# Optimization experiments

Measured on AMD Instinct MI355X. Metric: run time of the kernel, lower is better.

The kernel has to match this reference:

```python
import jax, jax.numpy as jnp
import numpy as np

D_MODEL = 1024
NUM_HEADS = 16
HEAD_DIM = D_MODEL // NUM_HEADS


def setup_inputs() -> dict:
    key = jax.random.key(0)
    ks = jax.random.split(key, 11)
    B, S, D = 2, 2048, D_MODEL
    scale = 1.0 / np.sqrt(D)
    inp = {
        "q": jax.random.normal(ks[0], (B, S, D), dtype=jnp.float32),
        "k": jax.random.normal(ks[1], (B, S, D), dtype=jnp.float32),
        "v": jax.random.normal(ks[2], (B, S, D), dtype=jnp.float32),
        # torch nn.Linear weights are [out, in]; y = x @ W.T + b
        "Wq": jax.random.normal(ks[3], (D, D), dtype=jnp.float32) * scale,
        "bq": jnp.zeros((D,), dtype=jnp.float32),
        "Wk": jax.random.normal(ks[4], (D, D), dtype=jnp.float32) * scale,
        "bk": jnp.zeros((D,), dtype=jnp.float32),
        "Wv": jax.random.normal(ks[5], (D, D), dtype=jnp.float32) * scale,
        "bv": jnp.zeros((D,), dtype=jnp.float32),
        "Wo": jax.random.normal(ks[6], (D, D), dtype=jnp.float32) * scale,
        "bo": jnp.zeros((D,), dtype=jnp.float32),
    }
    return inp


def _split_heads(x):
    B, S, D = x.shape
    return x.reshape(B, S, NUM_HEADS, HEAD_DIM).transpose(0, 2, 1, 3)  # [B,H,S,hd]


def reference(q, k, v, Wq, bq, Wk, bk, Wv, bv, Wo, bo):
    B, S, D = q.shape
    qh = _split_heads(q @ Wq.T + bq)
    kh = _split_heads(k @ Wk.T + bk)
    vh = _split_heads(v @ Wv.T + bv)
    # scores: [B,H,S,S], causal mask, softmax
    scores = jnp.einsum("bhqd,bhkd->bhqk", qh, kh) / jnp.sqrt(
        jnp.asarray(HEAD_DIM, dtype=qh.dtype))
    causal = jnp.tril(jnp.ones((S, S), dtype=bool))
    scores = jnp.where(causal[None, None], scores, -jnp.inf)
    attn = jax.nn.softmax(scores, axis=-1)
    out = jnp.einsum("bhqk,bhkd->bhqd", attn, vh)  # [B,H,S,hd]
    out = out.transpose(0, 2, 1, 3).reshape(B, S, D)
    return out @ Wo.T + bo
```

## Files before the change

kernel.cpp:

```cpp
#include <hip/hip_runtime.h>
#include <hip/hip_bf16.h>
#include <cstdint>
#include <cstddef>

typedef __bf16 bf16;
typedef __bf16 bf16x2 __attribute__((ext_vector_type(2)));
typedef __bf16 bf16x4 __attribute__((ext_vector_type(4)));
typedef __bf16 bf16x8 __attribute__((ext_vector_type(8)));
typedef float f32x4 __attribute__((ext_vector_type(4)));
typedef float f32x16 __attribute__((ext_vector_type(16)));
typedef unsigned int u32x4 __attribute__((ext_vector_type(4)));

#define S_LEN 2048
#define DM 1024
#define NH 16
#define HD 64
#define NQKV (4096 * 1024)
#define NW (1024 * 1024)
#define QK_SCALE 0.18033688011112042f

__device__ __forceinline__ void gload_lds16(const bf16* g, bf16* l) {
  __builtin_amdgcn_global_load_lds(
      (const __attribute__((address_space(1))) void*)g,
      (__attribute__((address_space(3))) void*)l, 16, 0, 0);
}

__device__ __forceinline__ unsigned packbf(float lo, float hi) {
  bf16x2 t;
  t[0] = (bf16)lo;
  t[1] = (bf16)hi;
  return __builtin_bit_cast(unsigned, t);
}

__device__ __forceinline__ void pl32swap(unsigned& a, unsigned& b) {
#if __has_builtin(__builtin_amdgcn_permlane32_swap)
  auto r = __builtin_amdgcn_permlane32_swap((int)a, (int)b, false, false);
  a = (unsigned)r[0];
  b = (unsigned)r[1];
#else
  asm volatile("v_permlane32_swap_b32 %0, %1" : "+v"(a), "+v"(b));
#endif
}

__global__ __launch_bounds__(256) void cvt_all(
    const float* __restrict__ q, const float* __restrict__ k, const float* __restrict__ v,
    const float* __restrict__ Wq, const float* __restrict__ Wk, const float* __restrict__ Wv,
    const float* __restrict__ Wo, bf16* __restrict__ out) {
  const size_t i = ((size_t)blockIdx.x * 256 + threadIdx.x) * 8;
  const float* src;
  size_t off;
  if (i < (size_t)NQKV) { src = q; off = i; }
  else if (i < 2ull * NQKV) { src = k; off = i - NQKV; }
  else if (i < 3ull * NQKV) { src = v; off = i - 2ull * NQKV; }
  else {
    const size_t j = i - 3ull * NQKV;
    if (j < (size_t)NW) { src = Wq; off = j; }
    else if (j < 2ull * NW) { src = Wk; off = j - NW; }
    else if (j < 3ull * NW) { src = Wv; off = j - 2ull * NW; }
    else { src = Wo; off = j - 3ull * NW; }
  }
  const float4 a = *(const float4*)(src + off);
  const float4 b = *(const float4*)(src + off + 4);
  bf16x8 o;
  o[0] = (bf16)a.x; o[1] = (bf16)a.y; o[2] = (bf16)a.z; o[3] = (bf16)a.w;
  o[4] = (bf16)b.x; o[5] = (bf16)b.y; o[6] = (bf16)b.z; o[7] = (bf16)b.w;
  *(bf16x8*)(out + i) = o;
}

template <int MODE>
__global__ __launch_bounds__(256, 3) void gemm_bt(
    const bf16* __restrict__ A, const bf16* __restrict__ W,
    const float* __restrict__ bias0, const float* __restrict__ bias1,
    const float* __restrict__ bias2, void* __restrict__ Out,
    int M, int N, int K, float scale) {
  __shared__ __align__(16) bf16 sm[3 * 2 * 128 * 32];
  const int tid = threadIdx.x;
  const int lane = tid & 63, w = tid >> 6;
  const int wr = w >> 1, wc = w & 1;
  const int r16 = lane & 15, grp = lane >> 4;

  int flat = blockIdx.y * gridDim.x + blockIdx.x;
  const int cpx = (gridDim.x * gridDim.y) >> 3;
  flat = (flat & 7) * cpx + (flat >> 3);
  const int m0 = (flat / gridDim.x) * 128;
  const int n0 = (flat % gridDim.x) * 128;

  const int seg = n0 >> 10;
  const bf16* Ab = (MODE == 3) ? A + (size_t)seg * NQKV : A;

  f32x4 acc[4][4] = {};

  int stG[2], stL[2];
#pragma unroll
  for (int j = 0; j < 2; ++j) {
    const int lin = j * 256 + tid;
    const int row = lin >> 2;
    const int ch = (lin & 3) ^ (row & 3);
    stG[j] = row * K + ch * 8;
    stL[j] = lin * 8;
  }

#define GSTAGE(t, s)                                                           \
  {                                                                            \
    const int k0_ = (t) << 5;                                                  \
    bf16* as_ = sm + (s) * 8192;                                               \
    bf16* bs_ = as_ + 4096;                                                    \
    _Pragma("unroll") for (int j = 0; j < 2; ++j) {                            \
      gload_lds16(&Ab[(size_t)m0 * K + k0_ + stG[j]], &as_[stL[j]]);           \
      gload_lds16(&W[(size_t)n0 * K + k0_ + stG[j]], &bs_[stL[j]]);            \
    }                                                                          \
  }

  const int nk = K >> 5;
  GSTAGE(0, 0)
  GSTAGE(1, 1)

  int cur = 0;
  for (int t = 0; t < nk; ++t) {
    if (t + 1 < nk) asm volatile("s_waitcnt vmcnt(4)" ::: "memory");
    else            asm volatile("s_waitcnt vmcnt(0)" ::: "memory");
    __builtin_amdgcn_s_barrier();

    if (t + 2 < nk) {
      int nxt = cur + 2; if (nxt >= 3) nxt -= 3;
      GSTAGE(t + 2, nxt)
    }

    const char* Asl = (const char*)(sm + cur * 8192);
    const char* Bsl = Asl + 8192;
    {
      bf16x8 af[4], bfr[4];
#pragma unroll
      for (int m = 0; m < 4; ++m) {
        const int row = wr * 64 + m * 16 + r16;
        af[m] = *(const bf16x8*)(Asl + row * 64 + ((grp * 16) ^ ((row & 3) << 4)));
      }
#pragma unroll
      for (int n = 0; n < 4; ++n) {
        const int row = wc * 64 + n * 16 + r16;
        bfr[n] = *(const bf16x8*)(Bsl + row * 64 + ((grp * 16) ^ ((row & 3) << 4)));
      }
#pragma unroll
      for (int m = 0; m < 4; ++m)
#pragma unroll
        for (int n = 0; n < 4; ++n)
          acc[m][n] = __builtin_amdgcn_mfma_f32_16x16x32_bf16(af[m], bfr[n], acc[m][n], 0, 0, 0);
    }
    ++cur; if (cur == 3) cur = 0;
  }
#undef GSTAGE

  const float* bp = (MODE == 3) ? (seg == 0 ? bias0 : (seg == 1 ? bias1 : bias2)) : bias0;
  const float sc = (MODE == 3) ? (seg == 0 ? scale : 1.0f) : scale;

  if (MODE == 3 && seg == 2) {
    __syncthreads();
    bf16* T = sm + w * (32 * 76);
    const int b = (m0 + wr * 64) >> 11;
    const int srow0 = (m0 + wr * 64) & 2047;
    bf16* base2 = (bf16*)Out + 2 * (size_t)NQKV;
#pragma unroll
    for (int p = 0; p < 2; ++p) {
#pragma unroll
      for (int nn = 0; nn < 2; ++nn) {
        const int n = 2 * p + nn;
#pragma unroll
        for (int mq = 0; mq < 4; ++mq)
#pragma unroll
          for (int r = 0; r < 4; ++r) {
            const int d_l = nn * 16 + r16;
            const int s_l = mq * 16 + grp * 4 + r;
            const int cs = (n0 + wc * 64 + n * 16 + r16) & 1023;
            T[d_l * 76 + s_l] = (bf16)(acc[mq][n][r] + bp[cs]);
          }
      }
      __syncthreads();
#pragma unroll
      for (int j = 0; j < 4; ++j) {
        const int d_l = j * 8 + (lane >> 3);
        const int scnk = lane & 7;
        const uint2 lo = *(const uint2*)&T[d_l * 76 + scnk * 8];
        const uint2 hi = *(const uint2*)&T[d_l * 76 + scnk * 8 + 4];
        const int cs = (n0 + wc * 64 + p * 32 + d_l) & 1023;
        const int hh = cs >> 6, dd = cs & 63;
        bf16* dst = base2 + ((size_t)(b * NH + hh) * HD + dd) * S_LEN + srow0 + scnk * 8;
        uint4 val; val.x = lo.x; val.y = lo.y; val.z = hi.x; val.w = hi.y;
        *(uint4*)dst = val;
      }
      __syncthreads();
    }
    return;
  }

#pragma unroll
  for (int m = 0; m < 4; ++m) {
#pragma unroll
    for (int n = 0; n < 4; ++n) {
#pragma unroll
      for (int r = 0; r < 4; ++r) {
        const int row = m0 + wr * 64 + m * 16 + grp * 4 + r;
        const int col = n0 + wc * 64 + n * 16 + r16;
        const int cs = col & 1023;
        const float v = (acc[m][n][r] + bp[cs]) * sc;
        if (MODE == 3) {
          const int b = row >> 11, s = row & 2047, h = cs >> 6, d = cs & 63;
          bf16* base = (bf16*)Out + (size_t)seg * NQKV;
          base[((size_t)(b * NH + h) * S_LEN + s) * HD + d] = (bf16)v;
        } else {
          ((float*)Out)[(size_t)row * N + col] = v;
        }
      }
    }
  }
}

__global__ __launch_bounds__(256, 3) void attn_fwd13(
    const bf16* __restrict__ Qh, const bf16* __restrict__ Kh,
    const bf16* __restrict__ Vt, bf16* __restrict__ AO) {
  __shared__ __align__(16) bf16 Kl[3][64 * 64];
  __shared__ __align__(16) bf16 Vl[3][64 * 64];

  const int tid = threadIdx.x;
  const int lane = tid & 63, w = tid >> 6;
  const int q31 = lane & 31, h = lane >> 5;
  const int qh = w >> 1, kh = w & 1;
  const int koff = kh << 5;

  const int bid = blockIdx.x;
  const int xcd = bid & 7;
  const int within = bid >> 3;
  const int bh = xcd * 4 + (within & 3);
  const int c = 31 - (within >> 2);

  const bf16* Qb = Qh + (size_t)bh * S_LEN * HD;
  const bf16* Kb = Kh + (size_t)bh * S_LEN * HD;
  const bf16* Vb = Vt + (size_t)bh * HD * S_LEN;

  int stK[2], stV[2], stL[2];
#pragma unroll
  for (int i = 0; i < 2; ++i) {
    const int lin = i * 256 + tid;
    const int row = lin >> 3;
    const int colb = (lin & 7) * 16;
    const int scol = colb ^ ((row & 7) << 4);
    stK[i] = row * HD + (scol >> 1);
    stV[i] = row * S_LEN + (scol >> 1);
    stL[i] = lin * 8;
  }
  const int swz = (q31 & 7) << 4;

#define STAGE(t, buf)                                                          \
  {                                                                            \
    const bf16* kb_ = Kb + (size_t)(t) * 64 * HD;                              \
    const bf16* vb_ = Vb + (t) * 64;                                           \
    _Pragma("unroll") for (int i = 0; i < 2; ++i) {                            \
      gload_lds16(kb_ + stK[i], &Kl[buf][stL[i]]);                             \
      gload_lds16(vb_ + stV[i], &Vl[buf][stL[i]]);                             \
    }                                                                          \
  }

  {
    const int q0 = c << 6;
    const int nt = c + 1;
    const int q0w = q0 + (qh << 5);
    const int qg = q0w + q31;
    const int nt_w = (w == 1) ? nt - 1 : nt;
    const bool maskw = (w == 0) || (w == 3);

    bf16x8 qf[4];
#pragma unroll
    for (int ks = 0; ks < 4; ++ks)
      qf[ks] = *(const bf16x8*)&Qb[(size_t)qg * HD + ks * 16 + 8 * h];

    f32x16 acc0 = {}, acc1 = {};
    float m = -1e30f, l = 0.f;

    STAGE(0, 0)
    if (nt > 1) STAGE(1, 1)

    int cur = 0;
    for (int kt = 0; kt < nt; ++kt) {
      if (kt + 1 < nt) asm volatile("s_waitcnt vmcnt(4)" ::: "memory");
      else             asm volatile("s_waitcnt vmcnt(0)" ::: "memory");
      __builtin_amdgcn_s_barrier();

      if (kt + 2 < nt) {
        int nxt = cur + 2; if (nxt >= 3) nxt -= 3;
        STAGE(kt + 2, nxt)
      }

      if (kt < nt_w) {
        const bf16* KlC = &Kl[cur][0];
        const bf16* VlC = &Vl[cur][0];

        bf16x8 kf[4];
#pragma unroll
        for (int ks = 0; ks < 4; ++ks) {
          const int cc = (32 * ks + 16 * h) ^ swz;
          kf[ks] = *(const bf16x8*)((const char*)KlC + (koff + q31) * 128 + cc);
        }

        f32x16 p0 = {};
        __builtin_amdgcn_s_setprio(1);
#pragma unroll
        for (int ks = 0; ks < 4; ++ks)
          p0 = __builtin_amdgcn_mfma_f32_32x32x16_bf16(kf[ks], qf[ks], p0, 0, 0, 0);
        __builtin_amdgcn_s_setprio(0);

        bf16x8 vf[4];
#pragma unroll
        for (int ks = 0; ks < 2; ++ks)
#pragma unroll
          for (int db = 0; db < 2; ++db) {
            const int cc = (64 * kh + 32 * ks + 16 * h) ^ swz;
            vf[ks * 2 + db] =
                *(const bf16x8*)((const char*)VlC + (db * 32 + q31) * 128 + cc);
          }

        if (maskw && kt == nt - 1) {
#pragma unroll
          for (int r = 0; r < 16; ++r) {
            const int key = (kt << 6) + koff + (r & 3) + 8 * (r >> 2) + 4 * h;
            if (key > qg) p0[r] = -1e30f;
          }
        }
        float t_[16];
#pragma unroll
        for (int r = 0; r < 16; ++r) t_[r] = p0[r];
#pragma unroll
        for (int s = 8; s >= 1; s >>= 1)
#pragma unroll
          for (int r = 0; r < s; ++r) t_[r] = fmaxf(t_[r], t_[r + s]);
        const float pmax = fmaxf(t_[0], __shfl_xor(t_[0], 32));
        if (!__all(pmax - m <= 8.0f)) {
          const float mn = fmaxf(m, pmax);
          const float al = exp2f(m - mn);
          m = mn;
          l *= al;
#pragma unroll
          for (int r = 0; r < 16; ++r) { acc0[r] *= al; acc1[r] *= al; }
        }
        float sv[16];
#pragma unroll
        for (int r = 0; r < 16; ++r) {
          p0[r] = exp2f(p0[r] - m);
          sv[r] = p0[r];
        }
#pragma unroll
        for (int s = 8; s >= 1; s >>= 1)
#pragma unroll
          for (int r = 0; r < s; ++r) sv[r] += sv[r + s];
        l += sv[0] + __shfl_xor(sv[0], 32);

        unsigned wv[8];
#pragma unroll
        for (int mm = 0; mm < 8; ++mm)
          wv[mm] = packbf(p0[2 * mm], p0[2 * mm + 1]);
        pl32swap(wv[0], wv[2]);
        pl32swap(wv[1], wv[3]);
        pl32swap(wv[4], wv[6]);
        pl32swap(wv[5], wv[7]);

        __builtin_amdgcn_s_setprio(1);
        {
          u32x4 pu0 = {wv[0], wv[1], wv[2], wv[3]};
          const bf16x8 pf0 = __builtin_bit_cast(bf16x8, pu0);
          acc0 = __builtin_amdgcn_mfma_f32_32x32x16_bf16(vf[0], pf0, acc0, 0, 0, 0);
          acc1 = __builtin_amdgcn_mfma_f32_32x32x16_bf16(vf[1], pf0, acc1, 0, 0, 0);
          u32x4 pu1 = {wv[4], wv[5], wv[6], wv[7]};
          const bf16x8 pf1 = __builtin_bit_cast(bf16x8, pu1);
          acc0 = __builtin_amdgcn_mfma_f32_32x32x16_bf16(vf[2], pf1, acc0, 0, 0, 0);
          acc1 = __builtin_amdgcn_mfma_f32_32x32x16_bf16(vf[3], pf1, acc1, 0, 0, 0);
        }
        __builtin_amdgcn_s_setprio(0);
      }

      ++cur; if (cur == 3) cur = 0;
    }

    float* scr = (float*)&Kl[0][0];
    float* s = scr + (size_t)qh * (64 * 34) + lane * 34;
    __syncthreads();
    if (kh) {
#pragma unroll
      for (int r = 0; r < 16; ++r) { s[r] = acc0[r]; s[16 + r] = acc1[r]; }
      s[32] = m;
      s[33] = l;
    }
    __syncthreads();
    if (!kh) {
      const float m1 = s[32], l1 = s[33];
      const float mn = fmaxf(m, m1);
      const float a0 = exp2f(m - mn), a1 = exp2f(m1 - mn);
      const float linv = 1.0f / (a0 * l + a1 * l1);
      const int b = bh >> 4, hh = bh & 15;
      bf16* orow = AO + ((size_t)(b * S_LEN + qg)) * DM + hh * HD;
#pragma unroll
      for (int mm = 0; mm < 4; ++mm) {
        bf16x4 ov0, ov1;
#pragma unroll
        for (int t2 = 0; t2 < 4; ++t2) {
          ov0[t2] = (bf16)((a0 * acc0[4 * mm + t2] + a1 * s[4 * mm + t2]) * linv);
          ov1[t2] = (bf16)((a0 * acc1[4 * mm + t2] + a1 * s[16 + 4 * mm + t2]) * linv);
        }
        *(bf16x4*)&orow[8 * mm + 4 * h] = ov0;
        *(bf16x4*)&orow[32 + 8 * mm + 4 * h] = ov1;
      }
    }
  }
#undef STAGE
}

extern "C" void kernel_launch(void* const* d_in, const int* in_sizes, int n_in,
                              void* d_out, int out_size, void* d_ws, size_t ws_size,
                              hipStream_t stream) {
  const float* q  = (const float*)d_in[0];
  const float* k  = (const float*)d_in[1];
  const float* v  = (const float*)d_in[2];
  const float* Wq = (const float*)d_in[3];
  const float* bq = (const float*)d_in[4];
  const float* Wk = (const float*)d_in[5];
  const float* bk = (const float*)d_in[6];
  const float* Wv = (const float*)d_in[7];
  const float* bv = (const float*)d_in[8];
  const float* Wo = (const float*)d_in[9];
  const float* bo = (const float*)d_in[10];

  const int NTOK = 2 * S_LEN;

  bf16* qb  = (bf16*)d_ws;
  bf16* Wqb = qb + 3 * (size_t)NQKV;
  bf16* Wob = Wqb + 3 * (size_t)NW;
  bf16* Qh  = Wqb + 4 * (size_t)NW;
  bf16* Kh  = Qh + (size_t)NQKV;
  bf16* Vt  = Kh + (size_t)NQKV;
  bf16* AO  = Vt + (size_t)NQKV;

  const int cvt_blocks = (3 * NQKV + 4 * NW) / 8 / 256;
  cvt_all<<<cvt_blocks, 256, 0, stream>>>(q, k, v, Wq, Wk, Wv, Wo, qb);

  gemm_bt<3><<<dim3(3 * DM / 128, NTOK / 128), 256, 0, stream>>>(
      qb, Wqb, bq, bk, bv, Qh, NTOK, 3 * DM, DM, QK_SCALE);

  attn_fwd13<<<dim3(1024), 256, 0, stream>>>(Qh, Kh, Vt, AO);

  gemm_bt<2><<<dim3(DM / 128, NTOK / 128), 256, 0, stream>>>(
      AO, Wob, bo, bo, bo, d_out, NTOK, DM, DM, 1.0f);
}
```

Before: 110.1 us.

## Split QKV projection into its own kernel with 256x128 tiles

Separates the fused QKV projection GEMM from the output GEMM and gives it a larger 256-row by 128-column block tile, with 8x4 MFMA accumulators per wave. The larger tile raises arithmetic intensity and halves the grid. MFMA sections are bracketed with s_setprio, and the V-transpose epilogue is reworked for the wider tile. The cost is more registers and LDS per block: occupancy bounds drop from 3 to 2, and there are fewer blocks to fill the CUs.

```diff
diff --git a/kernel.cpp b/kernel.cpp
--- a/kernel.cpp
+++ b/kernel.cpp
@@ -67,12 +67,10 @@
   *(bf16x8*)(out + i) = o;
 }
 
-template <int MODE>
-__global__ __launch_bounds__(256, 3) void gemm_bt(
+__global__ __launch_bounds__(256, 3) void gemm_out(
     const bf16* __restrict__ A, const bf16* __restrict__ W,
-    const float* __restrict__ bias0, const float* __restrict__ bias1,
-    const float* __restrict__ bias2, void* __restrict__ Out,
-    int M, int N, int K, float scale) {
+    const float* __restrict__ bias0, float* __restrict__ Out,
+    int M, int N, int K) {
   __shared__ __align__(16) bf16 sm[3 * 2 * 128 * 32];
   const int tid = threadIdx.x;
   const int lane = tid & 63, w = tid >> 6;
@@ -84,9 +82,6 @@
   flat = (flat & 7) * cpx + (flat >> 3);
   const int m0 = (flat / gridDim.x) * 128;
   const int n0 = (flat % gridDim.x) * 128;
-
-  const int seg = n0 >> 10;
-  const bf16* Ab = (MODE == 3) ? A + (size_t)seg * NQKV : A;
 
   f32x4 acc[4][4] = {};
 
@@ -106,7 +101,7 @@
     bf16* as_ = sm + (s) * 8192;                                               \
     bf16* bs_ = as_ + 4096;                                                    \
     _Pragma("unroll") for (int j = 0; j < 2; ++j) {                            \
-      gload_lds16(&Ab[(size_t)m0 * K + k0_ + stG[j]], &as_[stL[j]]);           \
+      gload_lds16(&A[(size_t)m0 * K + k0_ + stG[j]], &as_[stL[j]]);            \
       gload_lds16(&W[(size_t)n0 * K + k0_ + stG[j]], &bs_[stL[j]]);            \
     }                                                                          \
   }
@@ -150,39 +145,144 @@
   }
 #undef GSTAGE
 
-  const float* bp = (MODE == 3) ? (seg == 0 ? bias0 : (seg == 1 ? bias1 : bias2)) : bias0;
-  const float sc = (MODE == 3) ? (seg == 0 ? scale : 1.0f) : scale;
-
-  if (MODE == 3 && seg == 2) {
+#pragma unroll
+  for (int m = 0; m < 4; ++m)
+#pragma unroll
+    for (int n = 0; n < 4; ++n)
+#pragma unroll
+      for (int r = 0; r < 4; ++r) {
+        const int row = m0 + wr * 64 + m * 16 + grp * 4 + r;
+        const int col = n0 + wc * 64 + n * 16 + r16;
+        Out[(size_t)row * N + col] = acc[m][n][r] + bias0[col & 1023];
+      }
+}
+
+__global__ __launch_bounds__(256, 2) void gemm_qkv(
+    const bf16* __restrict__ A, const bf16* __restrict__ W,
+    const float* __restrict__ bias0, const float* __restrict__ bias1,
+    const float* __restrict__ bias2, bf16* __restrict__ Out, int K) {
+  __shared__ __align__(16) bf16 sm[3 * 12288];
+  const int tid = threadIdx.x;
+  const int lane = tid & 63, w = tid >> 6;
+  const int wr = w >> 1, wc = w & 1;
+  const int r16 = lane & 15, grp = lane >> 4;
+
+  int flat = blockIdx.y * gridDim.x + blockIdx.x;
+  const int cpx = (gridDim.x * gridDim.y) >> 3;
+  flat = (flat & 7) * cpx + (flat >> 3);
+  const int m0 = (flat / gridDim.x) * 256;
+  const int n0 = (flat % gridDim.x) * 128;
+
+  const int seg = n0 >> 10;
+  const bf16* Ab = A + (size_t)seg * NQKV;
+
+  f32x4 acc[8][4] = {};
+
+  int stGA[4], stLA[4], stGB[2], stLB[2];
+#pragma unroll
+  for (int j = 0; j < 4; ++j) {
+    const int lin = j * 256 + tid;
+    const int row = lin >> 2;
+    const int ch = (lin & 3) ^ (row & 3);
+    stGA[j] = row * K + ch * 8;
+    stLA[j] = lin * 8;
+  }
+#pragma unroll
+  for (int j = 0; j < 2; ++j) {
+    const int lin = j * 256 + tid;
+    const int row = lin >> 2;
+    const int ch = (lin & 3) ^ (row & 3);
+    stGB[j] = row * K + ch * 8;
+    stLB[j] = lin * 8;
+  }
+
+#define QSTAGE(t, s)                                                           \
+  {                                                                            \
+    const int k0_ = (t) << 5;                                                  \
+    bf16* as_ = sm + (s) * 12288;                                              \
+    bf16* bs_ = as_ + 8192;                                                    \
+    _Pragma("unroll") for (int j = 0; j < 4; ++j)                              \
+      gload_lds16(&Ab[(size_t)m0 * K + k0_ + stGA[j]], &as_[stLA[j]]);         \
+    _Pragma("unroll") for (int j = 0; j < 2; ++j)                              \
+      gload_lds16(&W[(size_t)n0 * K + k0_ + stGB[j]], &bs_[stLB[j]]);          \
+  }
+
+  const int nk = K >> 5;
+  QSTAGE(0, 0)
+  QSTAGE(1, 1)
+
+  int cur = 0;
+  for (int t = 0; t < nk; ++t) {
+    if (t + 1 < nk) asm volatile("s_waitcnt vmcnt(6)" ::: "memory");
+    else            asm volatile("s_waitcnt vmcnt(0)" ::: "memory");
+    __builtin_amdgcn_s_barrier();
+
+    if (t + 2 < nk) {
+      int nxt = cur + 2; if (nxt >= 3) nxt -= 3;
+      QSTAGE(t + 2, nxt)
+    }
+
+    const char* Asl = (const char*)(sm + cur * 12288);
+    const char* Bsl = Asl + 16384;
+    {
+      bf16x8 af[8], bfr[4];
+#pragma unroll
+      for (int m = 0; m < 8; ++m) {
+        const int row = wr * 128 + m * 16 + r16;
+        af[m] = *(const bf16x8*)(Asl + row * 64 + ((grp * 16) ^ ((row & 3) << 4)));
+      }
+#pragma unroll
+      for (int n = 0; n < 4; ++n) {
+        const int row = wc * 64 + n * 16 + r16;
+        bfr[n] = *(const bf16x8*)(Bsl + row * 64 + ((grp * 16) ^ ((row & 3) << 4)));
+      }
+      __builtin_amdgcn_s_setprio(1);
+#pragma unroll
+      for (int m = 0; m < 8; ++m)
+#pragma unroll
+        for (int n = 0; n < 4; ++n)
+          acc[m][n] = __builtin_amdgcn_mfma_f32_16x16x32_bf16(af[m], bfr[n], acc[m][n], 0, 0, 0);
+      __builtin_amdgcn_s_setprio(0);
+    }
+    ++cur; if (cur == 3) cur = 0;
+  }
+#undef QSTAGE
+
+  const float* bp = (seg == 0 ? bias0 : (seg == 1 ? bias1 : bias2));
+  const float sc = (seg == 0 ? QK_SCALE : 1.0f);
+
+  if (seg == 2) {
     __syncthreads();
-    bf16* T = sm + w * (32 * 76);
-    const int b = (m0 + wr * 64) >> 11;
-    const int srow0 = (m0 + wr * 64) & 2047;
-    bf16* base2 = (bf16*)Out + 2 * (size_t)NQKV;
+    bf16* T = sm + w * (32 * 132);
+    const int srow_base = m0 + wr * 128;
+    const int b = srow_base >> 11;
+    const int srow0 = srow_base & 2047;
+    const int hh = ((n0 + wc * 64) & 1023) >> 6;
+    bf16* base2 = Out + 2 * (size_t)NQKV;
 #pragma unroll
     for (int p = 0; p < 2; ++p) {
 #pragma unroll
       for (int nn = 0; nn < 2; ++nn) {
         const int n = 2 * p + nn;
-#pragma unroll
-        for (int mq = 0; mq < 4; ++mq)
+        const int cs = (n0 + wc * 64 + n * 16 + r16) & 1023;
+        const float bb = bp[cs];
+#pragma unroll
+        for (int mq = 0; mq < 8; ++mq)
 #pragma unroll
           for (int r = 0; r < 4; ++r) {
             const int d_l = nn * 16 + r16;
             const int s_l = mq * 16 + grp * 4 + r;
-            const int cs = (n0 + wc * 64 + n * 16 + r16) & 1023;
-            T[d_l * 76 + s_l] = (bf16)(acc[mq][n][r] + bp[cs]);
+            T[d_l * 132 + s_l] = (bf16)(acc[mq][n][r] + bb);
           }
       }
       __syncthreads();
 #pragma unroll
-      for (int j = 0; j < 4; ++j) {
-        const int d_l = j * 8 + (lane >> 3);
-        const int scnk = lane & 7;
-        const uint2 lo = *(const uint2*)&T[d_l * 76 + scnk * 8];
-        const uint2 hi = *(const uint2*)&T[d_l * 76 + scnk * 8 + 4];
-        const int cs = (n0 + wc * 64 + p * 32 + d_l) & 1023;
-        const int hh = cs >> 6, dd = cs & 63;
+      for (int j = 0; j < 8; ++j) {
+        const int d_l = j * 4 + (lane >> 4);
+        const int scnk = lane & 15;
+        const uint2 lo = *(const uint2*)&T[d_l * 132 + scnk * 8];
+        const uint2 hi = *(const uint2*)&T[d_l * 132 + scnk * 8 + 4];
+        const int dd = p * 32 + d_l;
         bf16* dst = base2 + ((size_t)(b * NH + hh) * HD + dd) * S_LEN + srow0 + scnk * 8;
         uint4 val; val.x = lo.x; val.y = lo.y; val.z = hi.x; val.w = hi.y;
         *(uint4*)dst = val;
@@ -192,26 +292,20 @@
     return;
   }
 
-#pragma unroll
-  for (int m = 0; m < 4; ++m) {
-#pragma unroll
-    for (int n = 0; n < 4; ++n) {
+  bf16* base = Out + (size_t)seg * NQKV;
+#pragma unroll
+  for (int m = 0; m < 8; ++m)
+#pragma unroll
+    for (int n = 0; n < 4; ++n)
 #pragma unroll
       for (int r = 0; r < 4; ++r) {
-        const int row = m0 + wr * 64 + m * 16 + grp * 4 + r;
+        const int row = m0 + wr * 128 + m * 16 + grp * 4 + r;
         const int col = n0 + wc * 64 + n * 16 + r16;
         const int cs = col & 1023;
         const float v = (acc[m][n][r] + bp[cs]) * sc;
-        if (MODE == 3) {
-          const int b = row >> 11, s = row & 2047, h = cs >> 6, d = cs & 63;
-          bf16* base = (bf16*)Out + (size_t)seg * NQKV;
-          base[((size_t)(b * NH + h) * S_LEN + s) * HD + d] = (bf16)v;
-        } else {
-          ((float*)Out)[(size_t)row * N + col] = v;
-        }
-      }
-    }
-  }
+        const int b = row >> 11, s = row & 2047, h = cs >> 6, d = cs & 63;
+        base[((size_t)(b * NH + h) * S_LEN + s) * HD + d] = (bf16)v;
+      }
 }
 
 __global__ __launch_bounds__(256, 3) void attn_fwd13(
@@ -439,11 +533,11 @@
   const int cvt_blocks = (3 * NQKV + 4 * NW) / 8 / 256;
   cvt_all<<<cvt_blocks, 256, 0, stream>>>(q, k, v, Wq, Wk, Wv, Wo, qb);
 
-  gemm_bt<3><<<dim3(3 * DM / 128, NTOK / 128), 256, 0, stream>>>(
-      qb, Wqb, bq, bk, bv, Qh, NTOK, 3 * DM, DM, QK_SCALE);
+  gemm_qkv<<<dim3(3 * DM / 128, NTOK / 256), 256, 0, stream>>>(
+      qb, Wqb, bq, bk, bv, Qh, DM);
 
   attn_fwd13<<<dim3(1024), 256, 0, stream>>>(Qh, Kh, Vt, AO);
 
-  gemm_bt<2><<<dim3(DM / 128, NTOK / 128), 256, 0, stream>>>(
-      AO, Wob, bo, bo, bo, d_out, NTOK, DM, DM, 1.0f);
-}
+  gemm_out<<<dim3(DM / 128, NTOK / 128), 256, 0, stream>>>(
+      AO, Wob, bo, (float*)d_out, NTOK, DM, DM);
+}
```

Result: no change. 109.2 us (-0.8%).
